# Kernel tuning notes

Measured on AMD Instinct MI355X. Metric: run time of the kernel, lower is better.

The kernel has to match this reference:

```python
import jax, jax.numpy as jnp
import numpy as np

NUM_HEADS = 16
WINDOW = 128

def setup_inputs() -> dict:
    key = jax.random.key(0)
    ks = jax.random.split(key, 9)
    E, B, S = 1024, 2, 2048
    sc = 1.0 / np.sqrt(E)
    return {
        'x':  jax.random.normal(ks[0], (B, S, E), jnp.float32),
        'Wq': jax.random.normal(ks[1], (E, E), jnp.float32) * sc,
        'bq': jax.random.normal(ks[2], (E,), jnp.float32) * 0.02,
        'Wk': jax.random.normal(ks[3], (E, E), jnp.float32) * sc,
        'bk': jax.random.normal(ks[4], (E,), jnp.float32) * 0.02,
        'Wv': jax.random.normal(ks[5], (E, E), jnp.float32) * sc,
        'bv': jax.random.normal(ks[6], (E,), jnp.float32) * 0.02,
        'Wo': jax.random.normal(ks[7], (E, E), jnp.float32) * sc,
        'bo': jax.random.normal(ks[8], (E,), jnp.float32) * 0.02,
    }

def reference(x, Wq, bq, Wk, bk, Wv, bv, Wo, bo):
    B, S, E = x.shape
    H = NUM_HEADS
    D = E // H
    # projections -> [B, H, S, D]
    q = (x @ Wq + bq).reshape(B, S, H, D).transpose(0, 2, 1, 3)
    k = (x @ Wk + bk).reshape(B, S, H, D).transpose(0, 2, 1, 3)
    v = (x @ Wv + bv).reshape(B, S, H, D).transpose(0, 2, 1, 3)
    # dense scores [B, H, S, S]
    energy = jnp.einsum('bhqd,bhkd->bhqk', q, k)
    idx = jnp.arange(S)
    blocked = jnp.abs(idx[:, None] - idx[None, :]) > WINDOW  # True = outside band
    neg = jnp.finfo(jnp.float32).min
    energy = jnp.where(blocked[None, None], neg, energy)
    # note: original scales by sqrt(emb_size), not sqrt(head_dim)
    att = jax.nn.softmax(energy / jnp.sqrt(jnp.float32(E)), axis=-1)
    out = jnp.einsum('bhqk,bhkd->bhqd', att, v)
    out = out.transpose(0, 2, 1, 3).reshape(B, S, E)
    return out @ Wo + bo
```

## Files before the change

kernel.cpp:

```cpp
#include <hip/hip_runtime.h>

typedef unsigned short u16;
typedef unsigned int u32;
typedef __attribute__((ext_vector_type(8))) short bf16x8;
typedef __attribute__((ext_vector_type(4))) float f32x4;
typedef __attribute__((ext_vector_type(4))) unsigned int u32x4;
typedef __attribute__((ext_vector_type(4))) unsigned short u16x4;

#define DEV static __device__ __forceinline__

DEV u16 f2bf(float f) {
  unsigned u = __builtin_bit_cast(unsigned, f);
  u += 0x7FFFu + ((u >> 16) & 1u);
  return (u16)(u >> 16);
}

DEV u32 cvt_pk_bf16(float lo, float hi) {
  u32 d;
  asm("v_cvt_pk_bf16_f32 %0, %1, %2" : "=v"(d) : "v"(lo), "v"(hi));
  return d;
}

DEV void load_lds16(const void* g, void* l) {
  __builtin_amdgcn_global_load_lds(
      (const __attribute__((address_space(1))) unsigned int*)g,
      (__attribute__((address_space(3))) unsigned int*)l, 16, 0, 0);
}


__global__ void k_prep(const float* __restrict__ x,
                       const float* __restrict__ bq, const float* __restrict__ bk,
                       const float* __restrict__ bv,
                       const float* __restrict__ Wq, const float* __restrict__ Wk,
                       const float* __restrict__ Wv, const float* __restrict__ Wo,
                       u16* __restrict__ xb, u16* __restrict__ wtqkv,
                       u16* __restrict__ wto, float* __restrict__ bias) {
  const int tid = threadIdx.x;
  const int bid = blockIdx.x;
  if (bid < 4096) {
    __shared__ float t[32][33];
    const int wi = bid >> 10, inner = bid & 1023;
    const float* W = (wi == 0) ? Wq : (wi == 1) ? Wk : (wi == 2) ? Wv : Wo;
    u16* Wt = (wi == 3) ? wto : wtqkv + (size_t)wi * 1024 * 1024;
    const int tx = tid & 31, ty = tid >> 5;
    const int c0 = (inner & 31) * 32, r0 = (inner >> 5) * 32;
#pragma unroll
    for (int i = 0; i < 4; ++i)
      t[ty + i * 8][tx] = W[(size_t)(r0 + ty + i * 8) * 1024 + c0 + tx];
    __syncthreads();
#pragma unroll
    for (int i = 0; i < 4; ++i)
      Wt[(size_t)(c0 + ty + i * 8) * 1024 + r0 + tx] = f2bf(t[tx][ty + i * 8]);
  } else if (bid < 8192) {
    int i = ((bid - 4096) * 256 + tid) * 4;
    f32x4 v = *(const f32x4*)(x + i);
    u16x4 o;
#pragma unroll
    for (int j = 0; j < 4; ++j) o[j] = f2bf(v[j]);
    *(u16x4*)(xb + i) = o;
  } else {
    int i = (bid - 8192) * 256 + tid;
    float v = (i < 1024) ? bq[i] : (i < 2048) ? bk[i - 1024] : bv[i - 2048];
    bias[i] = v;
  }
}


template <typename CT>
__launch_bounds__(256) __global__
void k_gemm_bt(const u16* __restrict__ A, const u16* __restrict__ Bt,
               const float* __restrict__ bias, CT* __restrict__ C, int ldc,
               u16* __restrict__ vtp) {
  __shared__ __align__(16) u16 lA[128 * 32];
  __shared__ __align__(16) u16 lB[128 * 32];
  __shared__ __align__(16) float ep[4][16][68];
  const int tid = threadIdx.x;
  const int w = tid >> 6, lane = tid & 63, g = lane >> 4, n16 = lane & 15;
  const int wm = w >> 1, wn = w & 1;
  const int m0 = blockIdx.y * 128, n0 = blockIdx.x * 128;

  f32x4 acc[4][4] = {};
  for (int k0 = 0; k0 < 1024; k0 += 32) {
    __syncthreads();
#pragma unroll
    for (int r = 0; r < 2; ++r) {
      int c = r * 256 + tid;
      load_lds16(A + (size_t)(m0 + (c >> 2)) * 1024 + k0 + (c & 3) * 8, &lA[c * 8]);
      load_lds16(Bt + (size_t)(n0 + (c >> 2)) * 1024 + k0 + (c & 3) * 8, &lB[c * 8]);
    }
    __syncthreads();
    bf16x8 af[4], bfr[4];
#pragma unroll
    for (int i = 0; i < 4; ++i)
      af[i] = *(const bf16x8*)&lA[(wm * 64 + i * 16 + n16) * 32 + g * 8];
#pragma unroll
    for (int j = 0; j < 4; ++j)
      bfr[j] = *(const bf16x8*)&lB[(wn * 64 + j * 16 + n16) * 32 + g * 8];
#pragma unroll
    for (int i = 0; i < 4; ++i)
#pragma unroll
      for (int j = 0; j < 4; ++j)
        acc[i][j] = __builtin_amdgcn_mfma_f32_16x16x32_bf16(af[i], bfr[j], acc[i][j], 0, 0, 0);
  }

  const int m_base = m0 + wm * 64, n_base = n0 + wn * 64;
  bool vmode = false;
  if constexpr (sizeof(CT) == 2) vmode = (vtp != nullptr) && (n_base >= 2048);

#pragma unroll
  for (int i = 0; i < 4; ++i) {
#pragma unroll
    for (int j = 0; j < 4; ++j) {
      float bv = bias[n_base + j * 16 + n16];
#pragma unroll
      for (int jj = 0; jj < 4; ++jj)
        ep[w][g * 4 + jj][j * 16 + n16] = acc[i][j][jj] + bv;
    }
    asm volatile("s_waitcnt lgkmcnt(0)" ::: "memory");
    if (vmode) {
      const int hd = n_base - 2048;
      const int head = hd >> 6;
      const int m_row0 = m_base + i * 16;
      const int bb = m_row0 >> 11, s0 = m_row0 & 2047;
      union { u16 a[16]; u32x4 v[2]; } pk;
#pragma unroll
      for (int r = 0; r < 16; ++r) pk.a[r] = f2bf(ep[w][r][lane]);
      size_t vrow = ((size_t)(bb * 16 + head) * 64 + lane) * 2048 + s0;
      *(u32x4*)(vtp + vrow) = pk.v[0];
      *(u32x4*)(vtp + vrow + 8) = pk.v[1];
    } else {
#pragma unroll
      for (int p = 0; p < 4; ++p) {
        int row = p * 4 + g;
        f32x4 v = *(const f32x4*)&ep[w][row][n16 * 4];
        size_t off = (size_t)(m_base + i * 16 + row) * ldc + n_base + n16 * 4;
        if constexpr (sizeof(CT) == 2) {
          u16x4 o;
#pragma unroll
          for (int q = 0; q < 4; ++q) o[q] = f2bf(v[q]);
          *(u16x4*)(C + off) = o;
        } else {
          *(f32x4*)(C + off) = v;
        }
      }
    }
    asm volatile("s_waitcnt lgkmcnt(0)" ::: "memory");
  }
}


__launch_bounds__(256, 3) __global__
void k_attn(const u16* __restrict__ qkv, const u16* __restrict__ vt,
            u16* __restrict__ attn) {
  __shared__ __align__(16) u16 KV[20480];
  __shared__ __align__(16) u16 Ostg[4][16][64];
  const int tid = threadIdx.x;
  const int w = tid >> 6, lane = tid & 63, g = lane >> 4, n16 = lane & 15;
  const int bid = (blockIdx.x & 7) * 128 + (blockIdx.x >> 3);
  const int qt = bid & 31, h = (bid >> 5) & 15, b = bid >> 9;
  const int q0b = qt * 64;
  const int kvb = q0b - 128;
  const int q0 = q0b + w * 16;
  const int kv0 = q0 - 128;
  const int q = q0 + n16;
  const int bh = b * 16 + h;

  {
    const u16* kpart = qkv + (size_t)b * 2048 * 3072 + 1024 + h * 64;
#pragma unroll
    for (int i = 0; i < 10; ++i) {
      int c = i * 256 + tid;
      int r = c >> 3, cc = c & 7;
      int srcr = min(max(kvb + r, 0), 2047);
      load_lds16(kpart + (size_t)srcr * 3072 + (cc ^ (r & 7)) * 8, &KV[c * 8]);
    }
  }

  const size_t rowQ = (size_t)(b * 2048 + q) * 3072 + h * 64;
  bf16x8 qf0 = *(const bf16x8*)(qkv + rowQ + g * 8);
  bf16x8 qf1 = *(const bf16x8*)(qkv + rowQ + 32 + g * 8);
  __syncthreads();

  const int kbase = 8 * (n16 >> 2) + (n16 & 3);
  const int wrel = 16 * w;
  f32x4 sv[18];
#pragma unroll
  for (int t = 0; t < 18; ++t) {
    int kr = wrel + 32 * (t >> 1) + 4 * (t & 1) + kbase;
    int krl = min(kr, 319);
    int p = krl & 7;
    const u16* kp = &KV[krl * 64];
    bf16x8 kf0 = *(const bf16x8*)(kp + (g ^ p) * 8);
    bf16x8 kf1 = *(const bf16x8*)(kp + ((g + 4) ^ p) * 8);
    f32x4 s = {0.f, 0.f, 0.f, 0.f};
    s = __builtin_amdgcn_mfma_f32_16x16x32_bf16(kf0, qf0, s, 0, 0, 0);
    s = __builtin_amdgcn_mfma_f32_16x16x32_bf16(kf1, qf1, s, 0, 0, 0);
    sv[t] = s;
  }
  __syncthreads();

  {
    const u16* vpart = vt + (size_t)bh * 64 * 2048;
#pragma unroll
    for (int i = 0; i < 10; ++i) {
      int c = i * 256 + tid;
      int d = c / 40, cc = c - d * 40;
      int j = cc ^ (d & 7);
      int srck = min(max(kvb + j * 8, 0), 2040);
      load_lds16(vpart + (size_t)d * 2048 + srck, &KV[c * 8]);
    }
  }

  const float NEG = -__builtin_inff();
#pragma unroll
  for (int t = 0; t < 18; ++t) {
    int kb = kv0 + 32 * (t >> 1) + 4 * (t & 1) + 8 * g;
#pragma unroll
    for (int jj = 0; jj < 4; ++jj) {
      int k = kb + jj;
      bool ok = ((unsigned)k < 2048u) && ((unsigned)(q - k + 128) <= 256u);
      sv[t][jj] = ok ? sv[t][jj] : NEG;
    }
  }

  float mx = NEG;
#pragma unroll
  for (int t = 0; t < 18; ++t)
    mx = fmaxf(mx, fmaxf(fmaxf(sv[t][0], sv[t][1]), fmaxf(sv[t][2], sv[t][3])));
  mx = fmaxf(mx, __shfl_xor(mx, 16));
  mx = fmaxf(mx, __shfl_xor(mx, 32));

  const float c = 0.04508422017f;
  const float nmc = -mx * c;
  float sum = 0.f;
#pragma unroll
  for (int t = 0; t < 18; ++t)
#pragma unroll
    for (int jj = 0; jj < 4; ++jj) {
      float p = exp2f(fmaf(sv[t][jj], c, nmc));
      sv[t][jj] = p;
      sum += p;
    }
  sum += __shfl_xor(sum, 16);
  sum += __shfl_xor(sum, 32);
  const float inv = 1.f / sum;

  __syncthreads();

  f32x4 oacc[4] = {};
#pragma unroll
  for (int s = 0; s < 9; ++s) {
    union { u32 u[4]; bf16x8 v; } paf;
    paf.u[0] = cvt_pk_bf16(sv[2 * s][0], sv[2 * s][1]);
    paf.u[1] = cvt_pk_bf16(sv[2 * s][2], sv[2 * s][3]);
    paf.u[2] = cvt_pk_bf16(sv[2 * s + 1][0], sv[2 * s + 1][1]);
    paf.u[3] = cvt_pk_bf16(sv[2 * s + 1][2], sv[2 * s + 1][3]);
    int jc = min(2 * w + 4 * s + g, 39);
#pragma unroll
    for (int dt = 0; dt < 4; ++dt) {
      int d = dt * 16 + n16;
      bf16x8 vf = *(const bf16x8*)&KV[d * 320 + (jc ^ (d & 7)) * 8];
      oacc[dt] = __builtin_amdgcn_mfma_f32_16x16x32_bf16(paf.v, vf, oacc[dt], 0, 0, 0);
    }
  }

  float rs[4];
#pragma unroll
  for (int jj = 0; jj < 4; ++jj) rs[jj] = __shfl(inv, 4 * g + jj);

#pragma unroll
  for (int dt = 0; dt < 4; ++dt)
#pragma unroll
    for (int jj = 0; jj < 4; ++jj)
      Ostg[w][g * 4 + jj][dt * 16 + n16] = f2bf(oacc[dt][jj] * rs[jj]);
  asm volatile("s_waitcnt lgkmcnt(0)" ::: "memory");
#pragma unroll
  for (int p = 0; p < 2; ++p) {
    int fl = p * 512 + lane * 8;
    int row = fl >> 6, col = fl & 63;
    u32x4 v = *(const u32x4*)&Ostg[w][row][col];
    *(u32x4*)(attn + (size_t)(b * 2048 + q0 + row) * 1024 + h * 64 + col) = v;
  }
}


extern "C" void kernel_launch(void* const* d_in, const int* in_sizes, int n_in,
                              void* d_out, int out_size, void* d_ws, size_t ws_size,
                              hipStream_t stream) {
  const float* x  = (const float*)d_in[0];
  const float* Wq = (const float*)d_in[1];
  const float* bq = (const float*)d_in[2];
  const float* Wk = (const float*)d_in[3];
  const float* bk = (const float*)d_in[4];
  const float* Wv = (const float*)d_in[5];
  const float* bv = (const float*)d_in[6];
  const float* Wo = (const float*)d_in[7];
  const float* bo = (const float*)d_in[8];

  char* ws = (char*)d_ws;
  const size_t MB = 1ull << 20;
  u16*   xb    = (u16*)(ws + 0);
  u16*   wtqkv = (u16*)(ws + 8 * MB);
  u16*   wto   = (u16*)(ws + 14 * MB);
  float* bias  = (float*)(ws + 16 * MB);
  u16*   qkvb  = (u16*)(ws + 17 * MB);
  u16*   vtb   = (u16*)(ws + 41 * MB);
  u16*   attnb = (u16*)(ws + 0);

  k_prep<<<8204, 256, 0, stream>>>(x, bq, bk, bv, Wq, Wk, Wv, Wo,
                                   xb, wtqkv, wto, bias);
  k_gemm_bt<u16><<<dim3(24, 32), 256, 0, stream>>>(xb, wtqkv, bias, qkvb, 3072, vtb);
  k_attn<<<1024, 256, 0, stream>>>(qkvb, vtb, attnb);
  k_gemm_bt<float><<<dim3(8, 32), 256, 0, stream>>>(attnb, wto, bo, (float*)d_out, 1024,
                                                    nullptr);
}
```

Baseline: 89.75 us.

## Double-buffer GEMM LDS tiles with swizzled layout and prefetch next k-slice

```diff
diff --git a/kernel.cpp b/kernel.cpp
--- a/kernel.cpp
+++ b/kernel.cpp
@@ -71,37 +71,60 @@
 void k_gemm_bt(const u16* __restrict__ A, const u16* __restrict__ Bt,
                const float* __restrict__ bias, CT* __restrict__ C, int ldc,
                u16* __restrict__ vtp) {
-  __shared__ __align__(16) u16 lA[128 * 32];
-  __shared__ __align__(16) u16 lB[128 * 32];
+  __shared__ __align__(16) u16 lA[2][128 * 32];
+  __shared__ __align__(16) u16 lB[2][128 * 32];
   __shared__ __align__(16) float ep[4][16][68];
   const int tid = threadIdx.x;
   const int w = tid >> 6, lane = tid & 63, g = lane >> 4, n16 = lane & 15;
   const int wm = w >> 1, wn = w & 1;
   const int m0 = blockIdx.y * 128, n0 = blockIdx.x * 128;
 
+  const int c0 = tid, c1 = 256 + tid;
+  const int r0_ = c0 >> 2, r1_ = c1 >> 2;
+  const int sc0 = ((c0 & 3) ^ (r0_ & 3) ^ ((r0_ >> 2) & 3)) * 8;
+  const int sc1 = ((c1 & 3) ^ (r1_ & 3) ^ ((r1_ >> 2) & 3)) * 8;
+  const u16* Ar0 = A + (size_t)(m0 + r0_) * 1024 + sc0;
+  const u16* Ar1 = A + (size_t)(m0 + r1_) * 1024 + sc1;
+  const u16* Br0 = Bt + (size_t)(n0 + r0_) * 1024 + sc0;
+  const u16* Br1 = Bt + (size_t)(n0 + r1_) * 1024 + sc1;
+  const int xsw = (n16 & 3) ^ ((n16 >> 2) & 3);
+
+#define STAGE(buf, k0)                              \
+  do {                                              \
+    load_lds16(Ar0 + (k0), &lA[buf][c0 * 8]);       \
+    load_lds16(Ar1 + (k0), &lA[buf][c1 * 8]);       \
+    load_lds16(Br0 + (k0), &lB[buf][c0 * 8]);       \
+    load_lds16(Br1 + (k0), &lB[buf][c1 * 8]);       \
+  } while (0)
+
   f32x4 acc[4][4] = {};
-  for (int k0 = 0; k0 < 1024; k0 += 32) {
-    __syncthreads();
-#pragma unroll
-    for (int r = 0; r < 2; ++r) {
-      int c = r * 256 + tid;
-      load_lds16(A + (size_t)(m0 + (c >> 2)) * 1024 + k0 + (c & 3) * 8, &lA[c * 8]);
-      load_lds16(Bt + (size_t)(n0 + (c >> 2)) * 1024 + k0 + (c & 3) * 8, &lB[c * 8]);
-    }
-    __syncthreads();
+  STAGE(0, 0);
+  for (int t = 0; t < 32; ++t) {
+    const int cur = t & 1;
+    if (t < 31) {
+      STAGE(cur ^ 1, (t + 1) * 32);
+      asm volatile("s_waitcnt vmcnt(4)" ::: "memory");
+    } else {
+      asm volatile("s_waitcnt vmcnt(0)" ::: "memory");
+    }
+    __builtin_amdgcn_s_barrier();
     bf16x8 af[4], bfr[4];
 #pragma unroll
     for (int i = 0; i < 4; ++i)
-      af[i] = *(const bf16x8*)&lA[(wm * 64 + i * 16 + n16) * 32 + g * 8];
+      af[i] = *(const bf16x8*)&lA[cur][(wm * 64 + i * 16 + n16) * 32 + (g ^ xsw) * 8];
 #pragma unroll
     for (int j = 0; j < 4; ++j)
-      bfr[j] = *(const bf16x8*)&lB[(wn * 64 + j * 16 + n16) * 32 + g * 8];
+      bfr[j] = *(const bf16x8*)&lB[cur][(wn * 64 + j * 16 + n16) * 32 + (g ^ xsw) * 8];
+    __builtin_amdgcn_s_setprio(1);
 #pragma unroll
     for (int i = 0; i < 4; ++i)
 #pragma unroll
       for (int j = 0; j < 4; ++j)
         acc[i][j] = __builtin_amdgcn_mfma_f32_16x16x32_bf16(af[i], bfr[j], acc[i][j], 0, 0, 0);
-  }
+    __builtin_amdgcn_s_setprio(0);
+    __builtin_amdgcn_s_barrier();
+  }
+#undef STAGE
 
   const int m_base = m0 + wm * 64, n_base = n0 + wn * 64;
   bool vmode = false;
@@ -118,8 +141,7 @@
     }
     asm volatile("s_waitcnt lgkmcnt(0)" ::: "memory");
     if (vmode) {
-      const int hd = n_base - 2048;
-      const int head = hd >> 6;
+      const int head = (n_base - 2048) >> 6;
       const int m_row0 = m_base + i * 16;
       const int bb = m_row0 >> 11, s0 = m_row0 & 2047;
       union { u16 a[16]; u32x4 v[2]; } pk;
```

New measurement: 96.32 us. +7.3%, slower.

## Deepen GEMM K-tile to 64 with XOR-swizzled LDS and narrower output GEMM tiles

Applied to the files above, without the earlier changes.

```diff
diff --git a/kernel.cpp b/kernel.cpp
--- a/kernel.cpp
+++ b/kernel.cpp
@@ -66,51 +66,71 @@
 }
 
 
-template <typename CT>
+template <int BN, typename CT>
 __launch_bounds__(256) __global__
 void k_gemm_bt(const u16* __restrict__ A, const u16* __restrict__ Bt,
                const float* __restrict__ bias, CT* __restrict__ C, int ldc,
                u16* __restrict__ vtp) {
-  __shared__ __align__(16) u16 lA[128 * 32];
-  __shared__ __align__(16) u16 lB[128 * 32];
-  __shared__ __align__(16) float ep[4][16][68];
+  constexpr int BM = 128, BK = 64;
+  constexpr int NJ = BN / 32;
+  constexpr int EPW = BN / 2 + 4;
+  __shared__ __align__(16) char smem[(BM + BN) * BK * 2];
+  u16* lA = (u16*)smem;
+  u16* lB = (u16*)(smem + BM * BK * 2);
+  float (*ep)[16][EPW] = (float (*)[16][EPW])smem;
+
   const int tid = threadIdx.x;
   const int w = tid >> 6, lane = tid & 63, g = lane >> 4, n16 = lane & 15;
   const int wm = w >> 1, wn = w & 1;
-  const int m0 = blockIdx.y * 128, n0 = blockIdx.x * 128;
-
-  f32x4 acc[4][4] = {};
-  for (int k0 = 0; k0 < 1024; k0 += 32) {
+  const int m0 = blockIdx.y * BM, n0 = blockIdx.x * BN;
+
+  f32x4 acc[4][NJ] = {};
+  for (int t = 0; t < 16; ++t) {
+    if (t) __syncthreads();
+    const int k0 = t * 64;
+#pragma unroll
+    for (int r = 0; r < BM / 32; ++r) {
+      int s = r * 256 + tid;
+      int row = s >> 3, cc = (s & 7) ^ (row & 7);
+      load_lds16(A + (size_t)(m0 + row) * 1024 + k0 + cc * 8, lA + s * 8);
+    }
+#pragma unroll
+    for (int r = 0; r < BN / 32; ++r) {
+      int s = r * 256 + tid;
+      int row = s >> 3, cc = (s & 7) ^ (row & 7);
+      load_lds16(Bt + (size_t)(n0 + row) * 1024 + k0 + cc * 8, lB + s * 8);
+    }
     __syncthreads();
 #pragma unroll
-    for (int r = 0; r < 2; ++r) {
-      int c = r * 256 + tid;
-      load_lds16(A + (size_t)(m0 + (c >> 2)) * 1024 + k0 + (c & 3) * 8, &lA[c * 8]);
-      load_lds16(Bt + (size_t)(n0 + (c >> 2)) * 1024 + k0 + (c & 3) * 8, &lB[c * 8]);
-    }
-    __syncthreads();
-    bf16x8 af[4], bfr[4];
-#pragma unroll
-    for (int i = 0; i < 4; ++i)
-      af[i] = *(const bf16x8*)&lA[(wm * 64 + i * 16 + n16) * 32 + g * 8];
-#pragma unroll
-    for (int j = 0; j < 4; ++j)
-      bfr[j] = *(const bf16x8*)&lB[(wn * 64 + j * 16 + n16) * 32 + g * 8];
-#pragma unroll
-    for (int i = 0; i < 4; ++i)
-#pragma unroll
-      for (int j = 0; j < 4; ++j)
-        acc[i][j] = __builtin_amdgcn_mfma_f32_16x16x32_bf16(af[i], bfr[j], acc[i][j], 0, 0, 0);
-  }
-
-  const int m_base = m0 + wm * 64, n_base = n0 + wn * 64;
+    for (int kh = 0; kh < 2; ++kh) {
+      const int csel = ((kh * 4 + g) ^ (n16 & 7)) * 8;
+      bf16x8 af[4], bfr[NJ];
+#pragma unroll
+      for (int i = 0; i < 4; ++i)
+        af[i] = *(const bf16x8*)&lA[(wm * 64 + i * 16 + n16) * 64 + csel];
+#pragma unroll
+      for (int j = 0; j < NJ; ++j)
+        bfr[j] = *(const bf16x8*)&lB[(wn * (BN / 2) + j * 16 + n16) * 64 + csel];
+      __builtin_amdgcn_s_setprio(1);
+#pragma unroll
+      for (int i = 0; i < 4; ++i)
+#pragma unroll
+        for (int j = 0; j < NJ; ++j)
+          acc[i][j] = __builtin_amdgcn_mfma_f32_16x16x32_bf16(af[i], bfr[j], acc[i][j], 0, 0, 0);
+      __builtin_amdgcn_s_setprio(0);
+    }
+  }
+  __syncthreads();
+
+  const int m_base = m0 + wm * 64, n_base = n0 + wn * (BN / 2);
   bool vmode = false;
-  if constexpr (sizeof(CT) == 2) vmode = (vtp != nullptr) && (n_base >= 2048);
+  if constexpr (sizeof(CT) == 2 && BN == 128)
+    vmode = (vtp != nullptr) && (n_base >= 2048);
 
 #pragma unroll
   for (int i = 0; i < 4; ++i) {
 #pragma unroll
-    for (int j = 0; j < 4; ++j) {
+    for (int j = 0; j < NJ; ++j) {
       float bv = bias[n_base + j * 16 + n16];
 #pragma unroll
       for (int jj = 0; jj < 4; ++jj)
@@ -118,8 +138,7 @@
     }
     asm volatile("s_waitcnt lgkmcnt(0)" ::: "memory");
     if (vmode) {
-      const int hd = n_base - 2048;
-      const int head = hd >> 6;
+      const int head = (n_base - 2048) >> 6;
       const int m_row0 = m_base + i * 16;
       const int bb = m_row0 >> 11, s0 = m_row0 & 2047;
       union { u16 a[16]; u32x4 v[2]; } pk;
@@ -129,11 +148,14 @@
       *(u32x4*)(vtp + vrow) = pk.v[0];
       *(u32x4*)(vtp + vrow + 8) = pk.v[1];
     } else {
-#pragma unroll
-      for (int p = 0; p < 4; ++p) {
-        int row = p * 4 + g;
-        f32x4 v = *(const f32x4*)&ep[w][row][n16 * 4];
-        size_t off = (size_t)(m_base + i * 16 + row) * ldc + n_base + n16 * 4;
+      constexpr int CPR = BN / 8;
+      constexpr int P = 16 * CPR / 64;
+#pragma unroll
+      for (int p = 0; p < P; ++p) {
+        int fl = p * 64 + lane;
+        int row = fl / CPR, cc = (fl % CPR) * 4;
+        f32x4 v = *(const f32x4*)&ep[w][row][cc];
+        size_t off = (size_t)(m_base + i * 16 + row) * ldc + n_base + cc;
         if constexpr (sizeof(CT) == 2) {
           u16x4 o;
 #pragma unroll
@@ -309,8 +331,8 @@
 
   k_prep<<<8204, 256, 0, stream>>>(x, bq, bk, bv, Wq, Wk, Wv, Wo,
                                    xb, wtqkv, wto, bias);
-  k_gemm_bt<u16><<<dim3(24, 32), 256, 0, stream>>>(xb, wtqkv, bias, qkvb, 3072, vtb);
+  k_gemm_bt<128, u16><<<dim3(24, 32), 256, 0, stream>>>(xb, wtqkv, bias, qkvb, 3072, vtb);
   k_attn<<<1024, 256, 0, stream>>>(qkvb, vtb, attnb);
-  k_gemm_bt<float><<<dim3(8, 32), 256, 0, stream>>>(attnb, wto, bo, (float*)d_out, 1024,
-                                                    nullptr);
-}
+  k_gemm_bt<64, float><<<dim3(16, 32), 256, 0, stream>>>(attnb, wto, bo, (float*)d_out,
+                                                         1024, nullptr);
+}
```

New measurement: 78.68 us. -12.3%, faster.
